# Kernel tuning notes

Hardware: AMD Instinct MI355X
Metric: run time of the kernel (lower is better)

## Reference

```python
import jax, jax.numpy as jnp
import numpy as np

B, LAT = 8, 64
NS_IN = [256, 1024, 4096]      # input node count per layer (U[i].shape[-1])
NS_OUT = [1024, 4096, 16384]   # output node count per layer (U[i].shape[0])
CH = [64, 64, 32, 3]           # feature channels: after fc, after conv0, conv1, conv2
DEG = 16


def setup_inputs() -> dict:
    key = jax.random.key(0)
    ks = iter(jax.random.split(key, 32))
    s = lambda n: 1.0 / np.sqrt(n)
    inp = {}
    inp["latents"] = jax.random.normal(next(ks), (B, LAT), jnp.float32)
    inp["fc_W"] = jax.random.normal(next(ks), (LAT, NS_IN[0] * CH[0]), jnp.float32) * s(LAT)
    inp["fc_b"] = jnp.zeros((NS_IN[0] * CH[0],), jnp.float32)
    for i in range(3):
        inp[f"U{i}"] = jax.random.normal(next(ks), (NS_OUT[i], NS_IN[i]), jnp.float32) * s(NS_IN[i])
        inp[f"Ub{i}"] = jnp.zeros((NS_OUT[i], CH[i]), jnp.float32)
        inp[f"W{i}"] = jax.random.normal(next(ks), (CH[i], CH[i + 1]), jnp.float32) * s(CH[i])
        inp[f"b{i}"] = jnp.zeros((CH[i + 1],), jnp.float32)
        E = NS_OUT[i] * DEG
        inp[f"vals{i}"] = jax.random.uniform(next(ks), (E,), jnp.float32)
        inp[f"rows{i}"] = jax.random.randint(next(ks), (E,), 0, NS_OUT[i], jnp.int32)
        inp[f"cols{i}"] = jax.random.randint(next(ks), (E,), 0, NS_OUT[i], jnp.int32)
    return inp


def _gcn(feat, rows, cols, vals, W, b, n_nodes):
    # sparse adjacency message passing: out = relu(A @ feat @ W + b)
    def one(f):  # f: [N, C]
        msg = vals[:, None] * f[cols]                      # [E, C]
        return jax.ops.segment_sum(msg, rows, num_segments=n_nodes)
    agg = jax.vmap(one)(feat)                              # [B, N, C]
    return jax.nn.relu(agg @ W + b)


def reference(latents, fc_W, fc_b,
              U0, Ub0, U1, Ub1, U2, Ub2,
              W0, b0, W1, b1, W2, b2,
              vals0, vals1, vals2,
              rows0, cols0, rows1, cols1, rows2, cols2):
    feat = latents @ fc_W + fc_b                           # [B, N0*C0]
    feat = feat.reshape(-1, NS_IN[0], CH[0])               # [B, N0, C0]
    Us = [U0, U1, U2]; Ubs = [Ub0, Ub1, Ub2]
    Ws = [W0, W1, W2]; bs = [b0, b1, b2]
    rs = [rows0, rows1, rows2]; cs = [cols0, cols1, cols2]; vs = [vals0, vals1, vals2]
    for i in range(3):
        # learned upsampling matmul + bias (tf.matmul / tf.map_fn are the same batched matmul)
        feat = jnp.einsum('on,bnc->boc', Us[i], feat) + Ubs[i]
        feat = _gcn(feat, rs[i], cs[i], vs[i], Ws[i], bs[i], NS_OUT[i])
    return feat                                            # [B, 16384, 3]
```

## Files before the change

kernel.cpp:

```cpp
#include <hip/hip_runtime.h>
#include <cstdint>
#include <cstddef>

#define TPB 256
#define CAP 128

typedef __bf16 bf16x8 __attribute__((ext_vector_type(8)));
typedef float f32x4 __attribute__((ext_vector_type(4)));

union FragU { ushort u[8]; uint4 q; bf16x8 v; };

__device__ __forceinline__ ushort f2bf(float f)
{
    union { float f; uint32_t u; } v; v.f = f;
    uint32_t r = v.u + 0x7FFFu + ((v.u >> 16) & 1u);
    return (ushort)(r >> 16);
}

__global__ __launch_bounds__(TPB) void k_prep(
    const float* __restrict__ lat, const float* __restrict__ W,
    const float* __restrict__ bias, float* __restrict__ out,
    int* __restrict__ cnt)
{
    int bx = blockIdx.x;
    if (bx < 512) {
        int tid = bx * TPB + threadIdx.x;
        int c = tid & 63;
        int b = (tid >> 6) & 7;
        int n = tid >> 9;
        int j = n * 64 + c;
        float acc = bias[j];
        const float* lb = lat + b * 64;
#pragma unroll 16
        for (int l = 0; l < 64; ++l)
            acc = fmaf(lb[l], W[l * 16384 + j], acc);
        out[tid] = acc;
    } else {
        int tid = (bx - 512) * TPB + threadIdx.x;
        if (tid < 21504) cnt[tid] = 0;
    }
}

__global__ __launch_bounds__(TPB) void k_build(
    const int* __restrict__ r0, const int* __restrict__ c0, const float* __restrict__ v0,
    const int* __restrict__ r1, const int* __restrict__ c1, const float* __restrict__ v1,
    const int* __restrict__ r2, const int* __restrict__ c2, const float* __restrict__ v2,
    int* __restrict__ cnt, int* __restrict__ ccol, float* __restrict__ cval,
    const float* __restrict__ X, const float* __restrict__ W0,
    const float* __restrict__ Ub0,
    ushort* __restrict__ Fq, float* __restrict__ UbW)
{
    int bx = blockIdx.x;
    if (bx < 1344) {
        int e = bx * TPB + threadIdx.x;
        int node, col; float val;
        if (e < 16384)       { node = r0[e];                col = c0[e];  val = v0[e]; }
        else if (e < 81920)  { int l = e - 16384; node = 1024 + r1[l]; col = c1[l]; val = v1[l]; }
        else                 { int l = e - 81920; node = 5120 + r2[l]; col = c2[l]; val = v2[l]; }
        int pos = atomicAdd(&cnt[node], 1);
        ccol[(size_t)node * CAP + pos] = col;
        cval[(size_t)node * CAP + pos] = val;
    } else if (bx < 1856) {
        int tid = (bx - 1344) * TPB + threadIdx.x;
        int co = tid % 64;
        int nb = tid / 64;
        const float* x = X + (size_t)nb * 64;
        float acc = 0.f;
#pragma unroll
        for (int ci = 0; ci < 64; ++ci)
            acc = fmaf(x[ci], W0[ci * 64 + co], acc);
        int n = nb >> 3, bb = nb & 7;
        int col = bb * 64 + co;
        int ks = n >> 5, r = n & 31, kq = r >> 3, j = r & 7;
        int ct = col >> 4, cl = col & 15;
        size_t idx = ((((size_t)ct * (256 / 32) + ks) * 4 + kq) * 16 + cl) * 8 + j;
        Fq[idx] = f2bf(acc);
    } else {
        int tid = (bx - 1856) * TPB + threadIdx.x;
        if (tid >= 65536) return;
        int co = tid % 64;
        int row = tid / 64;
        const float* x = Ub0 + (size_t)row * 64;
        float acc = 0.f;
#pragma unroll
        for (int ci = 0; ci < 64; ++ci)
            acc = fmaf(x[ci], W0[ci * 64 + co], acc);
        UbW[tid] = acc;
    }
}

template<int BCIN, int CI, int CO, int COLS, int KF, int NR, int RBASE, int NBUB>
__global__ __launch_bounds__(TPB) void k_gf(
    const float* __restrict__ up, const int* __restrict__ cnt,
    const int* __restrict__ ccol, const float* __restrict__ cval,
    const float* __restrict__ bias, const float* __restrict__ W,
    const float* __restrict__ Ub,
    ushort* __restrict__ Fq, float* __restrict__ UbW)
{
    int bx = blockIdx.x;
    if (bx < NR) {
        __shared__ float feat[BCIN];
        __shared__ float Wl[CI * CO];
        const int tid = threadIdx.x;
        const int r = bx;
#pragma unroll
        for (int i = tid; i < CI * CO; i += TPB) Wl[i] = W[i];
        size_t p0 = (size_t)(RBASE + r) * CAP;
        size_t p1 = p0 + cnt[RBASE + r];
#pragma unroll
        for (int c = tid; c < BCIN; c += TPB) {
            float acc = 0.f;
            for (size_t p = p0; p < p1; ++p)
                acc = fmaf(cval[p], up[(size_t)ccol[p] * BCIN + c], acc);
            feat[c] = fmaxf(acc + bias[c % CI], 0.f);
        }
        __syncthreads();
        const int n = r;
        const int ks = n >> 5, rr = n & 31, kq = rr >> 3, j = rr & 7;
#pragma unroll
        for (int colp = tid; colp < COLS; colp += TPB) {
            float acc = 0.f;
            if (colp < 8 * CO) {
                int b = colp / CO, co = colp % CO;
                const float* fb = feat + b * CI;
#pragma unroll
                for (int ci = 0; ci < CI; ++ci)
                    acc = fmaf(fb[ci], Wl[ci * CO + co], acc);
            }
            int ct = colp >> 4, cl = colp & 15;
            size_t idx = ((((size_t)ct * (KF / 32) + ks) * 4 + kq) * 16 + cl) * 8 + j;
            Fq[idx] = f2bf(acc);
        }
    } else {
        int tid = (bx - NR) * TPB + threadIdx.x;
        if (tid >= NBUB * CO) return;
        int co = tid % CO;
        int row = tid / CO;
        const float* x = Ub + (size_t)row * CI;
        float acc = 0.f;
#pragma unroll
        for (int ci = 0; ci < CI; ++ci)
            acc = fmaf(x[ci], W[ci * CO + co], acc);
        UbW[tid] = acc;
    }
}

template<int K, int NTOT, int CO, int CF, int RF>
__global__ __launch_bounds__(TPB) void k_gemm_ws(
    const float* __restrict__ U, const ushort* __restrict__ Fq,
    const float* __restrict__ UbW, float* __restrict__ up)
{
    constexpr int KCH = K / 4;
    constexpr int KS = KCH / 32;
    constexpr int NC = CF * 16;
    constexpr int RED = RF * NC * 16;
    static_assert(KS % 2 == 0, "even k-steps");

    __shared__ float red[4][RED];

    const int tid = threadIdx.x;
    const int lane = tid & 63;
    const int w = tid >> 6;
    const int rowbase = blockIdx.x * (RF * 16);
    const int jt = blockIdx.y;
    const int kq = lane >> 4;
    const int m = lane & 15;

    const float* Ap[RF];
#pragma unroll
    for (int rf = 0; rf < RF; ++rf)
        Ap[rf] = U + (size_t)(rowbase + rf * 16 + m) * K + w * KCH + kq * 8;

    const ushort* Bp[CF];
#pragma unroll
    for (int cf = 0; cf < CF; ++cf)
        Bp[cf] = Fq + ((size_t)(jt * CF + cf) * (K / 32) + (size_t)w * KS) * 512
                 + lane * 8;

    f32x4 acc[RF][CF];
#pragma unroll
    for (int rf = 0; rf < RF; ++rf)
#pragma unroll
        for (int cf = 0; cf < CF; ++cf)
            acc[rf][cf] = (f32x4){0.f, 0.f, 0.f, 0.f};

    float4 a[2][RF][2];
    uint4  b[2][CF];

#define LOAD_STEP(S, t)                                                     \
    if ((t) < KS) {                                                         \
        _Pragma("unroll")                                                   \
        for (int rf = 0; rf < RF; ++rf) {                                   \
            a[S][rf][0] = *reinterpret_cast<const float4*>(Ap[rf] + (t) * 32);     \
            a[S][rf][1] = *reinterpret_cast<const float4*>(Ap[rf] + (t) * 32 + 4); \
        }                                                                   \
        _Pragma("unroll")                                                   \
        for (int cf = 0; cf < CF; ++cf)                                     \
            b[S][cf] = *reinterpret_cast<const uint4*>(Bp[cf] + (t) * 512); \
    }

#define COMP_STEP(S)                                                        \
    {                                                                       \
        _Pragma("unroll")                                                   \
        for (int rf = 0; rf < RF; ++rf) {                                   \
            const float* fa = reinterpret_cast<const float*>(&a[S][rf][0]); \
            bf16x8 av;                                                      \
            _Pragma("unroll")                                               \
            for (int j = 0; j < 8; ++j) av[j] = (__bf16)fa[j];              \
            _Pragma("unroll")                                               \
            for (int cf = 0; cf < CF; ++cf) {                               \
                FragU bfr; bfr.q = b[S][cf];                                \
                acc[rf][cf] = __builtin_amdgcn_mfma_f32_16x16x32_bf16(      \
                    av, bfr.v, acc[rf][cf], 0, 0, 0);                       \
            }                                                               \
        }                                                                   \
    }

    LOAD_STEP(0, 0)
#pragma unroll
    for (int t = 0; t < KS; t += 2) {
        LOAD_STEP(1, t + 1)
        COMP_STEP(0)
        LOAD_STEP(0, t + 2)
        COMP_STEP(1)
    }
#undef LOAD_STEP
#undef COMP_STEP

#pragma unroll
    for (int rf = 0; rf < RF; ++rf)
#pragma unroll
        for (int cf = 0; cf < CF; ++cf)
#pragma unroll
            for (int r = 0; r < 4; ++r)
                red[w][(rf * NC + cf * 16 + m) * 16 + kq * 4 + r] = acc[rf][cf][r];
    __syncthreads();

#pragma unroll
    for (int e = tid; e < RED; e += TPB) {
        int rf = e / (NC * 16);
        int rem = e - rf * (NC * 16);
        int col = rem >> 4, row = rem & 15;
        float v = red[0][e] + red[1][e] + red[2][e] + red[3][e];
        int gcol = jt * NC + col;
        int grow = rowbase + rf * 16 + row;
        if (gcol < NTOT)
            up[(size_t)grow * NTOT + gcol] =
                v + UbW[(size_t)grow * CO + gcol % CO];
    }
}

template<int BC, int CO, int NR, int RBASE>
__global__ __launch_bounds__(TPB) void k_gather_out(
    const float* __restrict__ up, const int* __restrict__ cnt,
    const int* __restrict__ ccol, const float* __restrict__ cval,
    const float* __restrict__ bias, float* __restrict__ out)
{
    constexpr int JQ = BC / 4;
    int tid = blockIdx.x * TPB + threadIdx.x;
    if (tid >= NR * JQ) return;
    int jq = tid % JQ;
    int r = tid / JQ;
    size_t p0 = (size_t)(RBASE + r) * CAP;
    size_t p1 = p0 + cnt[RBASE + r];
    float4 acc = make_float4(0.f, 0.f, 0.f, 0.f);
    for (size_t p = p0; p < p1; ++p) {
        float v = cval[p];
        int c = ccol[p];
        float4 u = *reinterpret_cast<const float4*>(&up[(size_t)c * BC + jq * 4]);
        acc.x = fmaf(v, u.x, acc.x);
        acc.y = fmaf(v, u.y, acc.y);
        acc.z = fmaf(v, u.z, acc.z);
        acc.w = fmaf(v, u.w, acc.w);
    }
    int col0 = jq * 4;
    float a[4] = {acc.x, acc.y, acc.z, acc.w};
#pragma unroll
    for (int e = 0; e < 4; ++e) {
        int col = col0 + e;
        int b = col / 3, j = col - b * 3;
        out[(size_t)b * 49152 + (size_t)r * 3 + j] = fmaxf(a[e] + bias[j], 0.f);
    }
}

extern "C" void kernel_launch(void* const* d_in, const int* in_sizes, int n_in,
                              void* d_out, int out_size, void* d_ws, size_t ws_size,
                              hipStream_t stream)
{
    const float* lat   = (const float*)d_in[0];
    const float* fcW   = (const float*)d_in[1];
    const float* fcb   = (const float*)d_in[2];
    const float* U0    = (const float*)d_in[3];
    const float* Ub0   = (const float*)d_in[4];
    const float* W0    = (const float*)d_in[5];
    const float* b0    = (const float*)d_in[6];
    const float* vals0 = (const float*)d_in[7];
    const int*   rows0 = (const int*)d_in[8];
    const int*   cols0 = (const int*)d_in[9];
    const float* U1    = (const float*)d_in[10];
    const float* Ub1   = (const float*)d_in[11];
    const float* W1    = (const float*)d_in[12];
    const float* b1    = (const float*)d_in[13];
    const float* vals1 = (const float*)d_in[14];
    const int*   rows1 = (const int*)d_in[15];
    const int*   cols1 = (const int*)d_in[16];
    const float* U2    = (const float*)d_in[17];
    const float* Ub2   = (const float*)d_in[18];
    const float* W2    = (const float*)d_in[19];
    const float* b2    = (const float*)d_in[20];
    const float* vals2 = (const float*)d_in[21];
    const int*   rows2 = (const int*)d_in[22];
    const int*   cols2 = (const int*)d_in[23];

    float* ws = (float*)d_ws;
    float* fbuf0 = ws;
    float* fWq   = fbuf0 + 131072;
    float* UbW   = fWq   + 262144;
    float* up    = UbW   + 131072;
    int*   cnt   = (int*)(up + 1048576);
    int*   ccol  = cnt + 21760;
    float* cval  = (float*)(ccol + 2752512);

    ushort* Fq16 = (ushort*)fWq;
    float* out = (float*)d_out;

    hipLaunchKernelGGL(k_prep, dim3(596), dim3(TPB), 0, stream, lat, fcW, fcb, fbuf0, cnt);
    hipLaunchKernelGGL(k_build, dim3(2112), dim3(TPB), 0, stream,
                       rows0, cols0, vals0, rows1, cols1, vals1, rows2, cols2, vals2,
                       cnt, ccol, cval, fbuf0, W0, Ub0, Fq16, UbW);
    hipLaunchKernelGGL((k_gemm_ws<256, 512, 64, 8, 1>), dim3(64, 4), dim3(TPB), 0, stream,
                       U0, Fq16, UbW, up);
    hipLaunchKernelGGL((k_gf<512, 64, 32, 256, 1024, 1024, 0, 4096>), dim3(1536), dim3(TPB), 0, stream,
                       up, cnt, ccol, cval, b0, W1, Ub1, Fq16, UbW);
    hipLaunchKernelGGL((k_gemm_ws<1024, 256, 32, 8, 1>), dim3(256, 2), dim3(TPB), 0, stream,
                       U1, Fq16, UbW, up);
    hipLaunchKernelGGL((k_gf<256, 32, 3, 32, 4096, 4096, 1024, 16384>), dim3(4288), dim3(TPB), 0, stream,
                       up, cnt, ccol, cval, b1, W2, Ub2, Fq16, UbW);
    hipLaunchKernelGGL((k_gemm_ws<4096, 24, 3, 2, 2>), dim3(512, 1), dim3(TPB), 0, stream,
                       U2, Fq16, UbW, up);
    hipLaunchKernelGGL((k_gather_out<24, 3, 16384, 5120>), dim3(384), dim3(TPB), 0, stream,
                       up, cnt, ccol, cval, b2, out);
}
```

Baseline: 165.3 us.

## Pack edge col/val into int2 and process multiple nodes per block in gather

Edge lists are now stored as interleaved int2 (column, value bits) so each edge is fetched with a single 8-byte load instead of two separate arrays. The k_gf gather kernel gains an NPB parameter, so one block can handle several nodes, each with a slice of threads holding per-thread register accumulators. The second layer uses 8 nodes per block, which cuts the block count from 4288 to 704 and avoids idle threads when BCIN is 256. Each thread now walks its edge list once for several channels rather than re-reading the edge list per channel.

```diff
diff --git a/kernel.cpp b/kernel.cpp
--- a/kernel.cpp
+++ b/kernel.cpp
@@ -45,7 +45,7 @@
     const int* __restrict__ r0, const int* __restrict__ c0, const float* __restrict__ v0,
     const int* __restrict__ r1, const int* __restrict__ c1, const float* __restrict__ v1,
     const int* __restrict__ r2, const int* __restrict__ c2, const float* __restrict__ v2,
-    int* __restrict__ cnt, int* __restrict__ ccol, float* __restrict__ cval,
+    int* __restrict__ cnt, int2* __restrict__ ecv,
     const float* __restrict__ X, const float* __restrict__ W0,
     const float* __restrict__ Ub0,
     ushort* __restrict__ Fq, float* __restrict__ UbW)
@@ -58,8 +58,7 @@
         else if (e < 81920)  { int l = e - 16384; node = 1024 + r1[l]; col = c1[l]; val = v1[l]; }
         else                 { int l = e - 81920; node = 5120 + r2[l]; col = c2[l]; val = v2[l]; }
         int pos = atomicAdd(&cnt[node], 1);
-        ccol[(size_t)node * CAP + pos] = col;
-        cval[(size_t)node * CAP + pos] = val;
+        ecv[(size_t)node * CAP + pos] = make_int2(col, __float_as_int(val));
     } else if (bx < 1856) {
         int tid = (bx - 1344) * TPB + threadIdx.x;
         int co = tid % 64;
@@ -89,50 +88,69 @@
     }
 }
 
-template<int BCIN, int CI, int CO, int COLS, int KF, int NR, int RBASE, int NBUB>
+template<int NPB, int BCIN, int CI, int CO, int COLS, int KF,
+         int NNODE, int RBASE, int NBUB>
 __global__ __launch_bounds__(TPB) void k_gf(
     const float* __restrict__ up, const int* __restrict__ cnt,
-    const int* __restrict__ ccol, const float* __restrict__ cval,
+    const int2* __restrict__ ecv,
     const float* __restrict__ bias, const float* __restrict__ W,
     const float* __restrict__ Ub,
     ushort* __restrict__ Fq, float* __restrict__ UbW)
 {
+    constexpr int TPN = TPB / NPB;
+    constexpr int CPT = BCIN / TPN;
     int bx = blockIdx.x;
-    if (bx < NR) {
-        __shared__ float feat[BCIN];
+    if (bx < NNODE / NPB) {
+        __shared__ float feat[NPB * BCIN];
         __shared__ float Wl[CI * CO];
         const int tid = threadIdx.x;
-        const int r = bx;
 #pragma unroll
         for (int i = tid; i < CI * CO; i += TPB) Wl[i] = W[i];
-        size_t p0 = (size_t)(RBASE + r) * CAP;
-        size_t p1 = p0 + cnt[RBASE + r];
-#pragma unroll
-        for (int c = tid; c < BCIN; c += TPB) {
-            float acc = 0.f;
-            for (size_t p = p0; p < p1; ++p)
-                acc = fmaf(cval[p], up[(size_t)ccol[p] * BCIN + c], acc);
-            feat[c] = fmaxf(acc + bias[c % CI], 0.f);
+
+        const int ni = tid / TPN;
+        const int li = tid % TPN;
+        const int node = bx * NPB + ni;
+        const int deg = cnt[RBASE + node];
+        const int2* ep = ecv + (size_t)(RBASE + node) * CAP;
+
+        float acc[CPT];
+#pragma unroll
+        for (int k = 0; k < CPT; ++k) acc[k] = 0.f;
+        for (int p = 0; p < deg; ++p) {
+            int2 cv = ep[p];
+            float v = __int_as_float(cv.y);
+            const float* ur = up + (size_t)cv.x * BCIN + li;
+#pragma unroll
+            for (int k = 0; k < CPT; ++k)
+                acc[k] = fmaf(v, ur[k * TPN], acc[k]);
+        }
+#pragma unroll
+        for (int k = 0; k < CPT; ++k) {
+            int c = li + k * TPN;
+            feat[ni * BCIN + c] = fmaxf(acc[k] + bias[c % CI], 0.f);
         }
         __syncthreads();
-        const int n = r;
-        const int ks = n >> 5, rr = n & 31, kq = rr >> 3, j = rr & 7;
-#pragma unroll
-        for (int colp = tid; colp < COLS; colp += TPB) {
-            float acc = 0.f;
+
+#pragma unroll
+        for (int e = tid; e < NPB * COLS; e += TPB) {
+            int fni = e / COLS;
+            int colp = e % COLS;
+            int n = bx * NPB + fni;
+            float a = 0.f;
             if (colp < 8 * CO) {
                 int b = colp / CO, co = colp % CO;
-                const float* fb = feat + b * CI;
+                const float* fb = feat + fni * BCIN + b * CI;
 #pragma unroll
                 for (int ci = 0; ci < CI; ++ci)
-                    acc = fmaf(fb[ci], Wl[ci * CO + co], acc);
+                    a = fmaf(fb[ci], Wl[ci * CO + co], a);
             }
+            int ks = n >> 5, rr = n & 31, kq = rr >> 3, j = rr & 7;
             int ct = colp >> 4, cl = colp & 15;
             size_t idx = ((((size_t)ct * (KF / 32) + ks) * 4 + kq) * 16 + cl) * 8 + j;
-            Fq[idx] = f2bf(acc);
+            Fq[idx] = f2bf(a);
         }
     } else {
-        int tid = (bx - NR) * TPB + threadIdx.x;
+        int tid = (bx - NNODE / NPB) * TPB + threadIdx.x;
         if (tid >= NBUB * CO) return;
         int co = tid % CO;
         int row = tid / CO;
@@ -253,7 +271,7 @@
 template<int BC, int CO, int NR, int RBASE>
 __global__ __launch_bounds__(TPB) void k_gather_out(
     const float* __restrict__ up, const int* __restrict__ cnt,
-    const int* __restrict__ ccol, const float* __restrict__ cval,
+    const int2* __restrict__ ecv,
     const float* __restrict__ bias, float* __restrict__ out)
 {
     constexpr int JQ = BC / 4;
@@ -261,13 +279,13 @@
     if (tid >= NR * JQ) return;
     int jq = tid % JQ;
     int r = tid / JQ;
-    size_t p0 = (size_t)(RBASE + r) * CAP;
-    size_t p1 = p0 + cnt[RBASE + r];
+    int deg = cnt[RBASE + r];
+    const int2* ep = ecv + (size_t)(RBASE + r) * CAP;
     float4 acc = make_float4(0.f, 0.f, 0.f, 0.f);
-    for (size_t p = p0; p < p1; ++p) {
-        float v = cval[p];
-        int c = ccol[p];
-        float4 u = *reinterpret_cast<const float4*>(&up[(size_t)c * BC + jq * 4]);
+    for (int p = 0; p < deg; ++p) {
+        int2 cv = ep[p];
+        float v = __int_as_float(cv.y);
+        float4 u = *reinterpret_cast<const float4*>(&up[(size_t)cv.x * BC + jq * 4]);
         acc.x = fmaf(v, u.x, acc.x);
         acc.y = fmaf(v, u.y, acc.y);
         acc.z = fmaf(v, u.z, acc.z);
@@ -318,8 +336,7 @@
     float* UbW   = fWq   + 262144;
     float* up    = UbW   + 131072;
     int*   cnt   = (int*)(up + 1048576);
-    int*   ccol  = cnt + 21760;
-    float* cval  = (float*)(ccol + 2752512);
+    int2*  ecv   = (int2*)(cnt + 21764);
 
     ushort* Fq16 = (ushort*)fWq;
     float* out = (float*)d_out;
@@ -327,17 +344,19 @@
     hipLaunchKernelGGL(k_prep, dim3(596), dim3(TPB), 0, stream, lat, fcW, fcb, fbuf0, cnt);
     hipLaunchKernelGGL(k_build, dim3(2112), dim3(TPB), 0, stream,
                        rows0, cols0, vals0, rows1, cols1, vals1, rows2, cols2, vals2,
-                       cnt, ccol, cval, fbuf0, W0, Ub0, Fq16, UbW);
+                       cnt, ecv, fbuf0, W0, Ub0, Fq16, UbW);
     hipLaunchKernelGGL((k_gemm_ws<256, 512, 64, 8, 1>), dim3(64, 4), dim3(TPB), 0, stream,
                        U0, Fq16, UbW, up);
-    hipLaunchKernelGGL((k_gf<512, 64, 32, 256, 1024, 1024, 0, 4096>), dim3(1536), dim3(TPB), 0, stream,
-                       up, cnt, ccol, cval, b0, W1, Ub1, Fq16, UbW);
+    hipLaunchKernelGGL((k_gf<1, 512, 64, 32, 256, 1024, 1024, 0, 4096>),
+                       dim3(1536), dim3(TPB), 0, stream,
+                       up, cnt, ecv, b0, W1, Ub1, Fq16, UbW);
     hipLaunchKernelGGL((k_gemm_ws<1024, 256, 32, 8, 1>), dim3(256, 2), dim3(TPB), 0, stream,
                        U1, Fq16, UbW, up);
-    hipLaunchKernelGGL((k_gf<256, 32, 3, 32, 4096, 4096, 1024, 16384>), dim3(4288), dim3(TPB), 0, stream,
-                       up, cnt, ccol, cval, b1, W2, Ub2, Fq16, UbW);
+    hipLaunchKernelGGL((k_gf<8, 256, 32, 3, 32, 4096, 4096, 1024, 16384>),
+                       dim3(704), dim3(TPB), 0, stream,
+                       up, cnt, ecv, b1, W2, Ub2, Fq16, UbW);
     hipLaunchKernelGGL((k_gemm_ws<4096, 24, 3, 2, 2>), dim3(512, 1), dim3(TPB), 0, stream,
                        U2, Fq16, UbW, up);
     hipLaunchKernelGGL((k_gather_out<24, 3, 16384, 5120>), dim3(384), dim3(TPB), 0, stream,
-                       up, cnt, ccol, cval, b2, out);
-}
+                       up, cnt, ecv, b2, out);
+}
```

Measured after the change: 153.1 us, median of 2. -7.4%, faster.
